# Kernel tuning notes

Measured on AMD Instinct MI355X. Metric: run time of the kernel, lower is better.

## Reference

```python
import jax, jax.numpy as jnp
import numpy as np

TOP_K = 8


def setup_inputs() -> dict:
    key = jax.random.key(0)
    ks = jax.random.split(key, 5)
    B, S, H, E, I = 2, 1024, 2048, 64, 768
    return {
        "hidden_states": jax.random.normal(ks[0], (B, S, H), dtype=jnp.float32),
        "router_w": jax.random.normal(ks[1], (H, E), dtype=jnp.float32) * 0.02,
        "gate_w": jax.random.normal(ks[2], (E, H, I), dtype=jnp.float32) * 0.02,
        "up_w": jax.random.normal(ks[3], (E, H, I), dtype=jnp.float32) * 0.02,
        "down_w": jax.random.normal(ks[4], (E, I, H), dtype=jnp.float32) * 0.02,
    }


def reference(hidden_states, router_w, gate_w, up_w, down_w):
    B, S, H = hidden_states.shape
    E = router_w.shape[1]
    x = hidden_states.reshape(-1, H)                      # [T, H]
    T = x.shape[0]

    router_logits = x @ router_w                           # [T, E]
    probs = jax.nn.softmax(router_logits.astype(jnp.float32), axis=-1)
    topk_w, topk_idx = jax.lax.top_k(probs, TOP_K)         # [T, K]
    topk_w = topk_w / jnp.sum(topk_w, axis=-1, keepdims=True)  # norm_topk_prob
    topk_w = topk_w.astype(x.dtype)

    # Dense combine weights: zero for non-selected experts -> same math as the
    # gather/scatter loop, jit-friendly (no data-dependent shapes).
    combine = jnp.zeros((T, E), dtype=x.dtype)
    combine = combine.at[jnp.arange(T)[:, None], topk_idx].set(topk_w)  # [T, E]

    g = jnp.einsum('th,ehi->tei', x, gate_w)               # [T, E, I]
    u = jnp.einsum('th,ehi->tei', x, up_w)                 # [T, E, I]
    h = jax.nn.silu(g) * u                                 # SwiGLU
    out = jnp.einsum('te,tei,eih->th', combine, h, down_w)  # weighted combine

    return out.reshape(B, S, H), router_logits
```

## Files before the change

kernel.cpp:

```cpp
#include <hip/hip_runtime.h>
#include <hip/hip_bf16.h>

typedef __hip_bfloat16 bf16;
typedef short s16x8 __attribute__((ext_vector_type(8)));
typedef unsigned short u16x8 __attribute__((ext_vector_type(8)));
typedef float f32x4 __attribute__((ext_vector_type(4)));

#define T_TOK 2048
#define HDIM  2048
#define NEXP  64
#define IDIM  768
#define TOPK  8
#define OUT_OFF (T_TOK * HDIM)
#define NPAIR (T_TOK * TOPK)

#define WS_TOPK_IDX  0
#define WS_TOPK_W    (64 * 1024)
#define WS_PAIR_TOK  (128 * 1024)
#define WS_SLOT_OF   (192 * 1024)
#define WS_COUNTS    (256 * 1024)
#define WS_OFFSETS   (257 * 1024)
#define WS_CURSOR    (258 * 1024)
#define WS_H         (1024 * 1024)
#define WS_PARTIAL   (WS_H + (size_t)NPAIR * IDIM * 2)
#define WS_XB        WS_PARTIAL

__device__ __forceinline__ float bf_to_f(unsigned short u) {
    return __uint_as_float(((unsigned int)u) << 16);
}
__device__ __forceinline__ unsigned short f2bf(float f) {
    unsigned int u = __float_as_uint(f);
    unsigned int r = (u + 0x7FFFu + ((u >> 16) & 1u)) >> 16;
    return (unsigned short)r;
}
__device__ __forceinline__ unsigned cvtpk(float lo, float hi) {
    unsigned r;
    asm("v_cvt_pk_bf16_f32 %0, %1, %2" : "=v"(r) : "v"(lo), "v"(hi));
    return r;
}

typedef const __attribute__((address_space(1))) unsigned int* gas_ptr;
typedef __attribute__((address_space(3))) unsigned int* las_ptr;
__device__ __forceinline__ void gload_lds16(const void* g, void* l) {
    __builtin_amdgcn_global_load_lds((gas_ptr)g, (las_ptr)l, 16, 0, 0);
}

__global__ __launch_bounds__(256) void xbf_kernel(const float* __restrict__ x,
                                                  unsigned short* __restrict__ xb) {
    int i = blockIdx.x * 256 + threadIdx.x;
    const float4* src = (const float4*)x + (size_t)i * 2;
    float4 a = src[0], b = src[1];
    u16x8 o;
    o[0] = f2bf(a.x); o[1] = f2bf(a.y); o[2] = f2bf(a.z); o[3] = f2bf(a.w);
    o[4] = f2bf(b.x); o[5] = f2bf(b.y); o[6] = f2bf(b.z); o[7] = f2bf(b.w);
    ((u16x8*)xb)[i] = o;
}

__global__ __launch_bounds__(256) void router_kernel(
    const float* __restrict__ x, const float* __restrict__ rw,
    float* __restrict__ logits) {
    int wave = threadIdx.x >> 6;
    int lane = threadIdx.x & 63;
    int t = blockIdx.x * 4 + wave;
    const float4* x4 = (const float4*)(x + (size_t)t * HDIM);
    float acc = 0.f;
    for (int h4 = 0; h4 < HDIM / 4; ++h4) {
        float4 xv = x4[h4];
        int h = h4 * 4;
        acc = fmaf(xv.x, rw[(h + 0) * NEXP + lane], acc);
        acc = fmaf(xv.y, rw[(h + 1) * NEXP + lane], acc);
        acc = fmaf(xv.z, rw[(h + 2) * NEXP + lane], acc);
        acc = fmaf(xv.w, rw[(h + 3) * NEXP + lane], acc);
    }
    logits[t * NEXP + lane] = acc;
}

__global__ __launch_bounds__(64) void topk_kernel(
    const float* __restrict__ logits, int* __restrict__ topk_idx,
    float* __restrict__ topk_w, int* __restrict__ counts) {
    int t = blockIdx.x;
    int lane = threadIdx.x;
    float lg = logits[t * NEXP + lane];
    float mx = lg;
    for (int off = 32; off; off >>= 1) mx = fmaxf(mx, __shfl_xor(mx, off));
    float ex = expf(lg - mx);
    float sum = ex;
    for (int off = 32; off; off >>= 1) sum += __shfl_xor(sum, off);
    float prob = ex / sum;

    float pr = prob;
    float myv = 0.f;
    int myidx = 0;
    float ksum = 0.f;
    for (int k = 0; k < TOPK; ++k) {
        float v = pr;
        int idx = lane;
        for (int off = 32; off; off >>= 1) {
            float ov = __shfl_xor(v, off);
            int oi = __shfl_xor(idx, off);
            if (ov > v || (ov == v && oi < idx)) { v = ov; idx = oi; }
        }
        ksum += v;
        if (lane == k) { myidx = idx; myv = v; }
        if (lane == idx) pr = -1.f;
    }
    if (lane < TOPK) {
        topk_idx[t * TOPK + lane] = myidx;
        topk_w[t * TOPK + lane] = myv / ksum;
        atomicAdd(&counts[myidx], 1);
    }
}

__global__ __launch_bounds__(64) void scan_kernel(
    const int* __restrict__ counts, int* __restrict__ offsets, int* __restrict__ cursor) {
    int lane = threadIdx.x;
    int c = counts[lane];
    int incl = c;
    for (int off = 1; off < 64; off <<= 1) {
        int tt = __shfl_up(incl, off);
        if (lane >= off) incl += tt;
    }
    offsets[lane] = incl - c;
    if (lane == 63) offsets[64] = incl;
    cursor[lane] = 0;
}

__global__ __launch_bounds__(256) void scatter_kernel(
    const int* __restrict__ topk_idx, const int* __restrict__ offsets,
    int* __restrict__ cursor, int* __restrict__ pair_token, int* __restrict__ slot_of) {
    int i = blockIdx.x * 256 + threadIdx.x;
    if (i >= NPAIR) return;
    int t = i >> 3;
    int e = topk_idx[i];
    int pos = atomicAdd(&cursor[e], 1);
    int slot = offsets[e] + pos;
    pair_token[slot] = t;
    slot_of[i] = slot;
}

#define BM   128
#define BKS  64
#define NKG  (HDIM / BKS)
#define NKD  (IDIM / BKS)

#define GU_STEP(KS, BV, P)                                                    \
  {                                                                           \
            \
    uint4 w0, w1;                                                             \
    w0.x = cvtpk(BV[0].x, BV[1].x); w0.y = cvtpk(BV[2].x, BV[3].x);           \
    w0.z = cvtpk(BV[4].x, BV[5].x); w0.w = cvtpk(BV[6].x, BV[7].x);           \
    w1.x = cvtpk(BV[0].y, BV[1].y); w1.y = cvtpk(BV[2].y, BV[3].y);           \
    w1.z = cvtpk(BV[4].y, BV[5].y); w1.w = cvtpk(BV[6].y, BV[7].y);           \
    *(uint4*)&Bgu[P][brow0 * BKS + bslot] = w0;                               \
    *(uint4*)&Bgu[P][(brow0 + 1) * BKS + bslot] = w1;                         \
    __builtin_amdgcn_sched_barrier(0);                                        \
    if ((KS) + 1 < NKG) {                                                     \
      asm volatile("s_waitcnt vmcnt(8) lgkmcnt(0)" ::: "memory");             \
    } else {                                                                  \
      asm volatile("s_waitcnt vmcnt(0) lgkmcnt(0)" ::: "memory");             \
    }                                                                         \
    __builtin_amdgcn_s_barrier();                                             \
    __builtin_amdgcn_sched_barrier(0);                                        \
        \
    if ((KS) + 1 < NKG) {                                                     \
      int h1 = ((KS) + 1) * BKS;                                              \
      gload_lds16(aq[0] + h1, &As[(P) ^ 1][(0 * 512 + tid) * 8]);             \
      gload_lds16(aq[1] + h1, &As[(P) ^ 1][(1 * 512 + tid) * 8]);             \
      __builtin_amdgcn_sched_barrier(0);                                      \
    }                                                                         \
    if ((KS) + 2 < NKG) {                                                     \
      int h2 = ((KS) + 2) * BKS;                                              \
      _Pragma("unroll")                                                       \
      for (int i = 0; i < 8; ++i)                                             \
        BV[i] = *(const float2*)(bsrc + (size_t)(h2 + i) * IDIM);             \
      __builtin_amdgcn_sched_barrier(0);                                      \
    }                                                                         \
                                                    \
    _Pragma("unroll")                                                         \
    for (int kk = 0; kk < 2; ++kk) {                                          \
      int jk = kk * 4 + lg4;                                                  \
      s16x8 a[4], bg, bu;                                                     \
      _Pragma("unroll")                                                       \
      for (int mr = 0; mr < 4; ++mr) {                                        \
        int r = wr * 64 + mr * 16 + l15;                                      \
        a[mr] = *(const s16x8*)&As[P][r * BKS + ((jk ^ (r & 7)) * 8)];        \
      }                                                                       \
      int rg = wc * 16 + l15;                                                 \
      int ru = 64 + rg;                                                       \
      bg = *(const s16x8*)&Bgu[P][rg * BKS + ((jk ^ ((rg >> 1) & 7)) * 8)];   \
      bu = *(const s16x8*)&Bgu[P][ru * BKS + ((jk ^ ((ru >> 1) & 7)) * 8)];   \
      _Pragma("unroll")                                                       \
      for (int mr = 0; mr < 4; ++mr) {                                        \
        accg[mr] = __builtin_amdgcn_mfma_f32_16x16x32_bf16(a[mr], bg, accg[mr], 0, 0, 0); \
        accu[mr] = __builtin_amdgcn_mfma_f32_16x16x32_bf16(a[mr], bu, accu[mr], 0, 0, 0); \
      }                                                                       \
    }                                                                         \
  }

__global__ __launch_bounds__(512, 4) void gateup_mfma(
    const unsigned short* __restrict__ xb, const float* __restrict__ gate_w,
    const float* __restrict__ up_w, const int* __restrict__ offsets,
    const int* __restrict__ pair_token, unsigned short* __restrict__ hbuf) {
    int e = blockIdx.x;
    int ntile = blockIdx.z;
    int off = offsets[e];
    int cnt = offsets[e + 1] - off;
    if (cnt <= 0) return;

    __shared__ unsigned short As[2][BM * BKS];
    __shared__ unsigned short Bgu[2][BM * BKS];
    __shared__ int toks[BM];

    int tid = threadIdx.x;
    int lane = tid & 63;
    int wr = (tid >> 6) >> 2, wc = (tid >> 6) & 3;
    int l15 = lane & 15, lg4 = lane >> 4;

    int mat = tid >> 8;
    int t8 = tid & 255;
    int nI2 = t8 & 31, kC = t8 >> 5;
    int brow0 = mat * 64 + nI2 * 2;
    int bslot = (kC ^ (nI2 & 7)) * 8;
    const float* bsrc = (mat ? up_w : gate_w) + (size_t)e * HDIM * IDIM
                        + (size_t)(kC * 8) * IDIM + ntile * 64 + nI2 * 2;

    for (int mt = blockIdx.y; mt * BM < cnt; mt += gridDim.y) {
        int m0 = mt * BM;
        if (tid < BM) {
            int p = m0 + tid;
            toks[tid] = pair_token[off + (p < cnt ? p : 0)];
        }
        __syncthreads();
        const unsigned short* aq[2];
        #pragma unroll
        for (int q = 0; q < 2; ++q) {
            int row = q * 64 + (tid >> 3);
            aq[q] = xb + (size_t)toks[row] * HDIM + (((tid & 7) ^ (row & 7)) * 8);
        }
        f32x4 accg[4] = {};
        f32x4 accu[4] = {};

        gload_lds16(aq[0], &As[0][(0 * 512 + tid) * 8]);
        gload_lds16(aq[1], &As[0][(1 * 512 + tid) * 8]);
        __builtin_amdgcn_sched_barrier(0);
        float2 BvA[8], BvB[8];
        #pragma unroll
        for (int i = 0; i < 8; ++i)
            BvA[i] = *(const float2*)(bsrc + (size_t)i * IDIM);
        __builtin_amdgcn_sched_barrier(0);
        #pragma unroll
        for (int i = 0; i < 8; ++i)
            BvB[i] = *(const float2*)(bsrc + (size_t)(BKS + i) * IDIM);
        __builtin_amdgcn_sched_barrier(0);

        for (int ks = 0; ks < NKG; ks += 2) {
            GU_STEP(ks, BvA, 0);
            GU_STEP(ks + 1, BvB, 1);
        }

        int col = ntile * 64 + wc * 16 + l15;
        #pragma unroll
        for (int mr = 0; mr < 4; ++mr) {
            #pragma unroll
            for (int reg = 0; reg < 4; ++reg) {
                int r = m0 + wr * 64 + mr * 16 + lg4 * 4 + reg;
                if (r < cnt) {
                    float g = accg[mr][reg];
                    float u = accu[mr][reg];
                    float hv = (g / (1.f + __expf(-g))) * u;
                    hbuf[(size_t)(off + r) * IDIM + col] = f2bf(hv);
                }
            }
        }
    }
}

#define DN_STEP(KS, BV, P)                                                    \
  {                                                                           \
    uint4 w0, w1;                                                             \
    w0.x = cvtpk(BV[0].x, BV[1].x); w0.y = cvtpk(BV[2].x, BV[3].x);           \
    w0.z = cvtpk(BV[4].x, BV[5].x); w0.w = cvtpk(BV[6].x, BV[7].x);           \
    w1.x = cvtpk(BV[0].y, BV[1].y); w1.y = cvtpk(BV[2].y, BV[3].y);           \
    w1.z = cvtpk(BV[4].y, BV[5].y); w1.w = cvtpk(BV[6].y, BV[7].y);           \
    *(uint4*)&Bd[P][brow0 * BKS + bslot] = w0;                                \
    *(uint4*)&Bd[P][(brow0 + 1) * BKS + bslot] = w1;                          \
    __builtin_amdgcn_sched_barrier(0);                                        \
    if ((KS) + 1 < NKD) {                                                     \
      asm volatile("s_waitcnt vmcnt(8) lgkmcnt(0)" ::: "memory");             \
    } else {                                                                  \
      asm volatile("s_waitcnt vmcnt(0) lgkmcnt(0)" ::: "memory");             \
    }                                                                         \
    __builtin_amdgcn_s_barrier();                                             \
    __builtin_amdgcn_sched_barrier(0);                                        \
    if ((KS) + 1 < NKD) {                                                     \
      int k1 = ((KS) + 1) * BKS;                                              \
      gload_lds16(aq[0] + k1, &As[(P) ^ 1][(0 * 512 + tid) * 8]);             \
      gload_lds16(aq[1] + k1, &As[(P) ^ 1][(1 * 512 + tid) * 8]);             \
      __builtin_amdgcn_sched_barrier(0);                                      \
    }                                                                         \
    if ((KS) + 2 < NKD) {                                                     \
      int k2 = ((KS) + 2) * BKS;                                              \
      _Pragma("unroll")                                                       \
      for (int i = 0; i < 8; ++i)                                             \
        BV[i] = *(const float2*)(bsrc + (size_t)(k2 + i) * HDIM);             \
      __builtin_amdgcn_sched_barrier(0);                                      \
    }                                                                         \
    _Pragma("unroll")                                                         \
    for (int kk = 0; kk < 2; ++kk) {                                          \
      int jk = kk * 4 + lg4;                                                  \
      s16x8 a[4], b[2];                                                       \
      _Pragma("unroll")                                                       \
      for (int mr = 0; mr < 4; ++mr) {                                        \
        int r = wr * 64 + mr * 16 + l15;                                      \
        a[mr] = *(const s16x8*)&As[P][r * BKS + ((jk ^ (r & 7)) * 8)];        \
      }                                                                       \
      _Pragma("unroll")                                                       \
      for (int nr = 0; nr < 2; ++nr) {                                        \
        int row = wc * 32 + nr * 16 + l15;                                    \
        b[nr] = *(const s16x8*)&Bd[P][row * BKS + ((jk ^ ((row >> 1) & 7)) * 8)]; \
      }                                                                       \
      _Pragma("unroll")                                                       \
      for (int mr = 0; mr < 4; ++mr)                                          \
        _Pragma("unroll")                                                     \
        for (int nr = 0; nr < 2; ++nr)                                        \
          acc[mr][nr] = __builtin_amdgcn_mfma_f32_16x16x32_bf16(a[mr], b[nr], acc[mr][nr], 0, 0, 0); \
    }                                                                         \
  }

__global__ __launch_bounds__(512, 4) void down_mfma(
    const unsigned short* __restrict__ hbuf, const float* __restrict__ down_w,
    const int* __restrict__ offsets, unsigned short* __restrict__ partial) {
    int e = blockIdx.x;
    int ntile = blockIdx.z;
    int off = offsets[e];
    int cnt = offsets[e + 1] - off;
    if (cnt <= 0) return;

    __shared__ unsigned short As[2][BM * BKS];
    __shared__ unsigned short Bd[2][BM * BKS];

    int tid = threadIdx.x;
    int lane = tid & 63;
    int wr = (tid >> 6) >> 2, wc = (tid >> 6) & 3;
    int l15 = lane & 15, lg4 = lane >> 4;

    int nI2 = tid & 63, kC = tid >> 6;
    int brow0 = nI2 * 2;
    int bslot = (kC ^ (nI2 & 7)) * 8;
    const float* bsrc = down_w + (size_t)e * IDIM * HDIM
                        + (size_t)(kC * 8) * HDIM + ntile * 128 + nI2 * 2;

    for (int mt = blockIdx.y; mt * BM < cnt; mt += gridDim.y) {
        int m0 = mt * BM;
        __syncthreads();
        const unsigned short* aq[2];
        #pragma unroll
        for (int q = 0; q < 2; ++q) {
            int row = q * 64 + (tid >> 3);
            int rr = m0 + row;
            if (rr >= cnt) rr = cnt - 1;
            aq[q] = hbuf + (size_t)(off + rr) * IDIM + (((tid & 7) ^ (row & 7)) * 8);
        }
        f32x4 acc[4][2] = {};

        gload_lds16(aq[0], &As[0][(0 * 512 + tid) * 8]);
        gload_lds16(aq[1], &As[0][(1 * 512 + tid) * 8]);
        __builtin_amdgcn_sched_barrier(0);
        float2 BvA[8], BvB[8];
        #pragma unroll
        for (int i = 0; i < 8; ++i)
            BvA[i] = *(const float2*)(bsrc + (size_t)i * HDIM);
        __builtin_amdgcn_sched_barrier(0);
        #pragma unroll
        for (int i = 0; i < 8; ++i)
            BvB[i] = *(const float2*)(bsrc + (size_t)(BKS + i) * HDIM);
        __builtin_amdgcn_sched_barrier(0);

        for (int ks = 0; ks < NKD; ks += 2) {
            DN_STEP(ks, BvA, 0);
            DN_STEP(ks + 1, BvB, 1);
        }

        #pragma unroll
        for (int mr = 0; mr < 4; ++mr)
            #pragma unroll
            for (int nr = 0; nr < 2; ++nr) {
                int col = ntile * 128 + wc * 32 + nr * 16 + l15;
                #pragma unroll
                for (int reg = 0; reg < 4; ++reg) {
                    int r = m0 + wr * 64 + mr * 16 + lg4 * 4 + reg;
                    if (r < cnt)
                        partial[(size_t)(off + r) * HDIM + col] = f2bf(acc[mr][nr][reg]);
                }
            }
    }
}

__global__ __launch_bounds__(256) void reduce_kernel(
    const unsigned short* __restrict__ partial, const int* __restrict__ slot_of,
    const float* __restrict__ topk_w, float* __restrict__ out) {
    int t = blockIdx.x;
    int j8 = threadIdx.x * 8;
    __shared__ int ss[8];
    __shared__ float sw[8];
    if (threadIdx.x < 8) {
        ss[threadIdx.x] = slot_of[t * TOPK + threadIdx.x];
        sw[threadIdx.x] = topk_w[t * TOPK + threadIdx.x];
    }
    __syncthreads();
    float acc[8] = {};
    #pragma unroll
    for (int k = 0; k < TOPK; ++k) {
        u16x8 v = *(const u16x8*)&partial[(size_t)ss[k] * HDIM + j8];
        float w = sw[k];
        #pragma unroll
        for (int i = 0; i < 8; ++i)
            acc[i] = fmaf(w, bf_to_f((unsigned short)v[i]), acc[i]);
    }
    float4 o0 = {acc[0], acc[1], acc[2], acc[3]};
    float4 o1 = {acc[4], acc[5], acc[6], acc[7]};
    *(float4*)&out[(size_t)t * HDIM + j8] = o0;
    *(float4*)&out[(size_t)t * HDIM + j8 + 4] = o1;
}

extern "C" void kernel_launch(void* const* d_in, const int* in_sizes, int n_in,
                              void* d_out, int out_size, void* d_ws, size_t ws_size,
                              hipStream_t stream) {
    const float* x  = (const float*)d_in[0];
    const float* rw = (const float*)d_in[1];
    const float* gw = (const float*)d_in[2];
    const float* uw = (const float*)d_in[3];
    const float* dw = (const float*)d_in[4];
    float* out = (float*)d_out;
    float* logits = out + OUT_OFF;

    char* ws = (char*)d_ws;
    int*   topk_idx   = (int*)(ws + WS_TOPK_IDX);
    float* topk_w     = (float*)(ws + WS_TOPK_W);
    int*   pair_token = (int*)(ws + WS_PAIR_TOK);
    int*   slot_of    = (int*)(ws + WS_SLOT_OF);
    int*   counts     = (int*)(ws + WS_COUNTS);
    int*   offsets    = (int*)(ws + WS_OFFSETS);
    int*   cursor     = (int*)(ws + WS_CURSOR);
    unsigned short* hbuf    = (unsigned short*)(ws + WS_H);
    unsigned short* partial = (unsigned short*)(ws + WS_PARTIAL);
    unsigned short* xb      = (unsigned short*)(ws + WS_XB);

    hipMemsetAsync(counts, 0, NEXP * sizeof(int), stream);
    xbf_kernel<<<T_TOK * HDIM / (256 * 8), 256, 0, stream>>>(x, xb);
    router_kernel<<<T_TOK / 4, 256, 0, stream>>>(x, rw, logits);
    topk_kernel<<<T_TOK, 64, 0, stream>>>(logits, topk_idx, topk_w, counts);
    scan_kernel<<<1, 64, 0, stream>>>(counts, offsets, cursor);
    scatter_kernel<<<NPAIR / 256, 256, 0, stream>>>(topk_idx, offsets, cursor, pair_token, slot_of);
    gateup_mfma<<<dim3(NEXP, 4, IDIM / 64), 512, 0, stream>>>(xb, gw, uw, offsets, pair_token, hbuf);
    down_mfma<<<dim3(NEXP, 4, HDIM / 128), 512, 0, stream>>>(hbuf, dw, offsets, partial);
    reduce_kernel<<<dim3(T_TOK, 1), 256, 0, stream>>>(partial, slot_of, topk_w, out);
}
```

Before: 736.8 us.

## Flatten MoE GEMM grids with XCD-aware block mapping and peel tail steps

Both expert GEMM kernels switch from a 3D grid to a 1D grid with a custom block-to-(expert, ntile, m-slice) mapping. Consecutive block ids now spread over 8 experts, which likely targets the round-robin XCD dispatch so blocks sharing an expert's weights land on the same die's L2. The m-slice count drops from 4 to 2, and the last two k-steps are peeled so the prefetch conditions become compile-time constants. Launch bounds go from 4 to 2 waves per SIMD, allowing more registers at the cost of occupancy, and a trailing __syncthreads is added in gateup between m-tiles.

```diff
diff --git a/kernel.cpp b/kernel.cpp
--- a/kernel.cpp
+++ b/kernel.cpp
@@ -142,10 +142,11 @@
 #define BKS  64
 #define NKG  (HDIM / BKS)
 #define NKD  (IDIM / BKS)
-
-#define GU_STEP(KS, BV, P)                                                    \
+#define SB() __builtin_amdgcn_sched_barrier(0)
+
+#define GU_STEP(KS, BV, P, DOA, DOB, WZ)                                      \
   {                                                                           \
-            \
+                        \
     uint4 w0, w1;                                                             \
     w0.x = cvtpk(BV[0].x, BV[1].x); w0.y = cvtpk(BV[2].x, BV[3].x);           \
     w0.z = cvtpk(BV[4].x, BV[5].x); w0.w = cvtpk(BV[6].x, BV[7].x);           \
@@ -153,27 +154,22 @@
     w1.z = cvtpk(BV[4].y, BV[5].y); w1.w = cvtpk(BV[6].y, BV[7].y);           \
     *(uint4*)&Bgu[P][brow0 * BKS + bslot] = w0;                               \
     *(uint4*)&Bgu[P][(brow0 + 1) * BKS + bslot] = w1;                         \
-    __builtin_amdgcn_sched_barrier(0);                                        \
-    if ((KS) + 1 < NKG) {                                                     \
-      asm volatile("s_waitcnt vmcnt(8) lgkmcnt(0)" ::: "memory");             \
-    } else {                                                                  \
-      asm volatile("s_waitcnt vmcnt(0) lgkmcnt(0)" ::: "memory");             \
-    }                                                                         \
+    SB();                                                                     \
+    if (WZ) { asm volatile("s_waitcnt vmcnt(0) lgkmcnt(0)" ::: "memory"); }   \
+    else    { asm volatile("s_waitcnt vmcnt(8) lgkmcnt(0)" ::: "memory"); }   \
     __builtin_amdgcn_s_barrier();                                             \
-    __builtin_amdgcn_sched_barrier(0);                                        \
-        \
-    if ((KS) + 1 < NKG) {                                                     \
+    SB();                                                                     \
+    if (DOA) {                                                                \
       int h1 = ((KS) + 1) * BKS;                                              \
-      gload_lds16(aq[0] + h1, &As[(P) ^ 1][(0 * 512 + tid) * 8]);             \
-      gload_lds16(aq[1] + h1, &As[(P) ^ 1][(1 * 512 + tid) * 8]);             \
-      __builtin_amdgcn_sched_barrier(0);                                      \
-    }                                                                         \
-    if ((KS) + 2 < NKG) {                                                     \
+      gload_lds16(aq[0] + h1, &As[(P) ^ 1][tid * 8]);                         \
+      gload_lds16(aq[1] + h1, &As[(P) ^ 1][(512 + tid) * 8]);                 \
+      SB();                                                                   \
+    }                                                                         \
+    if (DOB) {                                                                \
       int h2 = ((KS) + 2) * BKS;                                              \
       _Pragma("unroll")                                                       \
       for (int i = 0; i < 8; ++i)                                             \
         BV[i] = *(const float2*)(bsrc + (size_t)(h2 + i) * IDIM);             \
-      __builtin_amdgcn_sched_barrier(0);                                      \
     }                                                                         \
                                                     \
     _Pragma("unroll")                                                         \
@@ -197,12 +193,16 @@
     }                                                                         \
   }
 
-__global__ __launch_bounds__(512, 4) void gateup_mfma(
+__global__ __launch_bounds__(512, 2) void gateup_mfma(
     const unsigned short* __restrict__ xb, const float* __restrict__ gate_w,
     const float* __restrict__ up_w, const int* __restrict__ offsets,
     const int* __restrict__ pair_token, unsigned short* __restrict__ hbuf) {
-    int e = blockIdx.x;
-    int ntile = blockIdx.z;
+    int id = blockIdx.x;
+    int b = id & 7, r9 = id >> 3;
+    int y = r9 & 1;
+    int c = r9 >> 1;
+    int ntile = c >> 3;
+    int e = b + 8 * (c & 7);
     int off = offsets[e];
     int cnt = offsets[e + 1] - off;
     if (cnt <= 0) return;
@@ -224,7 +224,7 @@
     const float* bsrc = (mat ? up_w : gate_w) + (size_t)e * HDIM * IDIM
                         + (size_t)(kC * 8) * IDIM + ntile * 64 + nI2 * 2;
 
-    for (int mt = blockIdx.y; mt * BM < cnt; mt += gridDim.y) {
+    for (int mt = y; mt * BM < cnt; mt += 2) {
         int m0 = mt * BM;
         if (tid < BM) {
             int p = m0 + tid;
@@ -240,42 +240,45 @@
         f32x4 accg[4] = {};
         f32x4 accu[4] = {};
 
-        gload_lds16(aq[0], &As[0][(0 * 512 + tid) * 8]);
-        gload_lds16(aq[1], &As[0][(1 * 512 + tid) * 8]);
-        __builtin_amdgcn_sched_barrier(0);
+        gload_lds16(aq[0], &As[0][tid * 8]);
+        gload_lds16(aq[1], &As[0][(512 + tid) * 8]);
+        SB();
         float2 BvA[8], BvB[8];
         #pragma unroll
         for (int i = 0; i < 8; ++i)
             BvA[i] = *(const float2*)(bsrc + (size_t)i * IDIM);
-        __builtin_amdgcn_sched_barrier(0);
+        SB();
         #pragma unroll
         for (int i = 0; i < 8; ++i)
             BvB[i] = *(const float2*)(bsrc + (size_t)(BKS + i) * IDIM);
-        __builtin_amdgcn_sched_barrier(0);
-
-        for (int ks = 0; ks < NKG; ks += 2) {
-            GU_STEP(ks, BvA, 0);
-            GU_STEP(ks + 1, BvB, 1);
-        }
+        SB();
+
+        for (int ks = 0; ks < NKG - 2; ks += 2) {
+            GU_STEP(ks, BvA, 0, 1, 1, 0);
+            GU_STEP(ks + 1, BvB, 1, 1, 1, 0);
+        }
+        GU_STEP(NKG - 2, BvA, 0, 1, 0, 0);
+        GU_STEP(NKG - 1, BvB, 1, 0, 0, 1);
 
         int col = ntile * 64 + wc * 16 + l15;
         #pragma unroll
         for (int mr = 0; mr < 4; ++mr) {
             #pragma unroll
             for (int reg = 0; reg < 4; ++reg) {
-                int r = m0 + wr * 64 + mr * 16 + lg4 * 4 + reg;
-                if (r < cnt) {
+                int rr = m0 + wr * 64 + mr * 16 + lg4 * 4 + reg;
+                if (rr < cnt) {
                     float g = accg[mr][reg];
                     float u = accu[mr][reg];
                     float hv = (g / (1.f + __expf(-g))) * u;
-                    hbuf[(size_t)(off + r) * IDIM + col] = f2bf(hv);
+                    hbuf[(size_t)(off + rr) * IDIM + col] = f2bf(hv);
                 }
             }
         }
-    }
-}
-
-#define DN_STEP(KS, BV, P)                                                    \
+        __syncthreads();
+    }
+}
+
+#define DN_STEP(KS, BV, P, DOA, DOB, WZ)                                      \
   {                                                                           \
     uint4 w0, w1;                                                             \
     w0.x = cvtpk(BV[0].x, BV[1].x); w0.y = cvtpk(BV[2].x, BV[3].x);           \
@@ -284,31 +287,27 @@
     w1.z = cvtpk(BV[4].y, BV[5].y); w1.w = cvtpk(BV[6].y, BV[7].y);           \
     *(uint4*)&Bd[P][brow0 * BKS + bslot] = w0;                                \
     *(uint4*)&Bd[P][(brow0 + 1) * BKS + bslot] = w1;                          \
-    __builtin_amdgcn_sched_barrier(0);                                        \
-    if ((KS) + 1 < NKD) {                                                     \
-      asm volatile("s_waitcnt vmcnt(8) lgkmcnt(0)" ::: "memory");             \
-    } else {                                                                  \
-      asm volatile("s_waitcnt vmcnt(0) lgkmcnt(0)" ::: "memory");             \
-    }                                                                         \
+    SB();                                                                     \
+    if (WZ) { asm volatile("s_waitcnt vmcnt(0) lgkmcnt(0)" ::: "memory"); }   \
+    else    { asm volatile("s_waitcnt vmcnt(8) lgkmcnt(0)" ::: "memory"); }   \
     __builtin_amdgcn_s_barrier();                                             \
-    __builtin_amdgcn_sched_barrier(0);                                        \
-    if ((KS) + 1 < NKD) {                                                     \
+    SB();                                                                     \
+    if (DOA) {                                                                \
       int k1 = ((KS) + 1) * BKS;                                              \
-      gload_lds16(aq[0] + k1, &As[(P) ^ 1][(0 * 512 + tid) * 8]);             \
-      gload_lds16(aq[1] + k1, &As[(P) ^ 1][(1 * 512 + tid) * 8]);             \
-      __builtin_amdgcn_sched_barrier(0);                                      \
-    }                                                                         \
-    if ((KS) + 2 < NKD) {                                                     \
+      gload_lds16(aq[0] + k1, &As[(P) ^ 1][tid * 8]);                         \
+      gload_lds16(aq[1] + k1, &As[(P) ^ 1][(512 + tid) * 8]);                 \
+      SB();                                                                   \
+    }                                                                         \
+    if (DOB) {                                                                \
       int k2 = ((KS) + 2) * BKS;                                              \
       _Pragma("unroll")                                                       \
       for (int i = 0; i < 8; ++i)                                             \
         BV[i] = *(const float2*)(bsrc + (size_t)(k2 + i) * HDIM);             \
-      __builtin_amdgcn_sched_barrier(0);                                      \
     }                                                                         \
     _Pragma("unroll")                                                         \
     for (int kk = 0; kk < 2; ++kk) {                                          \
       int jk = kk * 4 + lg4;                                                  \
-      s16x8 a[4], b[2];                                                       \
+      s16x8 a[4], bb[2];                                                      \
       _Pragma("unroll")                                                       \
       for (int mr = 0; mr < 4; ++mr) {                                        \
         int r = wr * 64 + mr * 16 + l15;                                      \
@@ -317,21 +316,25 @@
       _Pragma("unroll")                                                       \
       for (int nr = 0; nr < 2; ++nr) {                                        \
         int row = wc * 32 + nr * 16 + l15;                                    \
-        b[nr] = *(const s16x8*)&Bd[P][row * BKS + ((jk ^ ((row >> 1) & 7)) * 8)]; \
+        bb[nr] = *(const s16x8*)&Bd[P][row * BKS + ((jk ^ ((row >> 1) & 7)) * 8)]; \
       }                                                                       \
       _Pragma("unroll")                                                       \
       for (int mr = 0; mr < 4; ++mr)                                          \
         _Pragma("unroll")                                                     \
         for (int nr = 0; nr < 2; ++nr)                                        \
-          acc[mr][nr] = __builtin_amdgcn_mfma_f32_16x16x32_bf16(a[mr], b[nr], acc[mr][nr], 0, 0, 0); \
+          acc[mr][nr] = __builtin_amdgcn_mfma_f32_16x16x32_bf16(a[mr], bb[nr], acc[mr][nr], 0, 0, 0); \
     }                                                                         \
   }
 
-__global__ __launch_bounds__(512, 4) void down_mfma(
+__global__ __launch_bounds__(512, 2) void down_mfma(
     const unsigned short* __restrict__ hbuf, const float* __restrict__ down_w,
     const int* __restrict__ offsets, unsigned short* __restrict__ partial) {
-    int e = blockIdx.x;
-    int ntile = blockIdx.z;
+    int id = blockIdx.x;
+    int b = id & 7, r9 = id >> 3;
+    int y = r9 & 1;
+    int c = r9 >> 1;
+    int ntile = c >> 3;
+    int e = b + 8 * (c & 7);
     int off = offsets[e];
     int cnt = offsets[e + 1] - off;
     if (cnt <= 0) return;
@@ -350,7 +353,7 @@
     const float* bsrc = down_w + (size_t)e * IDIM * HDIM
                         + (size_t)(kC * 8) * HDIM + ntile * 128 + nI2 * 2;
 
-    for (int mt = blockIdx.y; mt * BM < cnt; mt += gridDim.y) {
+    for (int mt = y; mt * BM < cnt; mt += 2) {
         int m0 = mt * BM;
         __syncthreads();
         const unsigned short* aq[2];
@@ -363,23 +366,25 @@
         }
         f32x4 acc[4][2] = {};
 
-        gload_lds16(aq[0], &As[0][(0 * 512 + tid) * 8]);
-        gload_lds16(aq[1], &As[0][(1 * 512 + tid) * 8]);
-        __builtin_amdgcn_sched_barrier(0);
+        gload_lds16(aq[0], &As[0][tid * 8]);
+        gload_lds16(aq[1], &As[0][(512 + tid) * 8]);
+        SB();
         float2 BvA[8], BvB[8];
         #pragma unroll
         for (int i = 0; i < 8; ++i)
             BvA[i] = *(const float2*)(bsrc + (size_t)i * HDIM);
-        __builtin_amdgcn_sched_barrier(0);
+        SB();
         #pragma unroll
         for (int i = 0; i < 8; ++i)
             BvB[i] = *(const float2*)(bsrc + (size_t)(BKS + i) * HDIM);
-        __builtin_amdgcn_sched_barrier(0);
-
-        for (int ks = 0; ks < NKD; ks += 2) {
-            DN_STEP(ks, BvA, 0);
-            DN_STEP(ks + 1, BvB, 1);
-        }
+        SB();
+
+        for (int ks = 0; ks < NKD - 2; ks += 2) {
+            DN_STEP(ks, BvA, 0, 1, 1, 0);
+            DN_STEP(ks + 1, BvB, 1, 1, 1, 0);
+        }
+        DN_STEP(NKD - 2, BvA, 0, 1, 0, 0);
+        DN_STEP(NKD - 1, BvB, 1, 0, 0, 1);
 
         #pragma unroll
         for (int mr = 0; mr < 4; ++mr)
@@ -388,9 +393,9 @@
                 int col = ntile * 128 + wc * 32 + nr * 16 + l15;
                 #pragma unroll
                 for (int reg = 0; reg < 4; ++reg) {
-                    int r = m0 + wr * 64 + mr * 16 + lg4 * 4 + reg;
-                    if (r < cnt)
-                        partial[(size_t)(off + r) * HDIM + col] = f2bf(acc[mr][nr][reg]);
+                    int rr = m0 + wr * 64 + mr * 16 + lg4 * 4 + reg;
+                    if (rr < cnt)
+                        partial[(size_t)(off + rr) * HDIM + col] = f2bf(acc[mr][nr][reg]);
                 }
             }
     }
@@ -452,7 +457,7 @@
     topk_kernel<<<T_TOK, 64, 0, stream>>>(logits, topk_idx, topk_w, counts);
     scan_kernel<<<1, 64, 0, stream>>>(counts, offsets, cursor);
     scatter_kernel<<<NPAIR / 256, 256, 0, stream>>>(topk_idx, offsets, cursor, pair_token, slot_of);
-    gateup_mfma<<<dim3(NEXP, 4, IDIM / 64), 512, 0, stream>>>(xb, gw, uw, offsets, pair_token, hbuf);
-    down_mfma<<<dim3(NEXP, 4, HDIM / 128), 512, 0, stream>>>(hbuf, dw, offsets, partial);
+    gateup_mfma<<<NEXP * 12 * 2, 512, 0, stream>>>(xb, gw, uw, offsets, pair_token, hbuf);
+    down_mfma<<<NEXP * 16 * 2, 512, 0, stream>>>(hbuf, dw, offsets, partial);
     reduce_kernel<<<dim3(T_TOK, 1), 256, 0, stream>>>(partial, slot_of, topk_w, out);
 }
```

New measurement: 871.3 us. 1.18x slower.
